# Kernel optimization log

Measured on AMD Instinct MI355X. Metric: run time of the kernel, lower is better.

The kernel has to match this reference:

```python
import jax, jax.numpy as jnp
import numpy as np

N_NODES = 100000


def setup_inputs() -> dict:
    key = jax.random.key(0)
    ks = jax.random.split(key, 7)
    n, d, c, e = N_NODES, 256, 128, 3200000
    features = jax.random.normal(ks[0], (n, d), dtype=jnp.float32)
    adj_row = jax.random.randint(ks[1], (e,), 0, n, dtype=jnp.int32)
    adj_col = jax.random.randint(ks[2], (e,), 0, n, dtype=jnp.int32)
    adj_vals = jax.random.uniform(ks[3], (e,), dtype=jnp.float32)
    kernel = jax.random.normal(ks[4], (d, c), dtype=jnp.float32) * (1.0 / np.sqrt(d))
    bias = jax.random.normal(ks[5], (c,), dtype=jnp.float32) * 0.01
    skip_weight = jax.random.normal(ks[6], (c,), dtype=jnp.float32)
    return {"features": features, "adj_row": adj_row, "adj_col": adj_col,
            "adj_vals": adj_vals, "kernel": kernel, "bias": bias,
            "skip_weight": skip_weight}


def reference(features, adj_row, adj_col, adj_vals, kernel, bias, skip_weight):
    # h = X @ W  : [n, c]
    h = features @ kernel
    # SpMM: out[r] += A[r, c] * h[c] over edges (COO)
    msgs = adj_vals[:, None] * h[adj_col]            # [e, c]
    agg = jax.ops.segment_sum(msgs, adj_row, num_segments=N_NODES)  # [n, c]
    out = h * skip_weight + agg                      # skip-connection scale + aggregation
    out = out + bias
    return jax.nn.selu(out)
```

## Files before the change

kernel.cpp:

```cpp
#include <hip/hip_runtime.h>
#include <math.h>

#define N_NODES 100000
#define D 256
#define C 128
#define N_EDGES 3200000

#define BROWS 128
#define NBUCKET ((N_NODES + BROWS - 1) / BROWS)
#define CAP 4608
#define EPB 8192
#define PBLOCKS ((N_EDGES + EPB - 1) / EPB)

#define GROWS 128
#define NGB ((N_NODES + GROWS - 1) / GROWS)
#define KH 128
#define XPAD 136

typedef __attribute__((ext_vector_type(8))) short bf16x8;
typedef __attribute__((ext_vector_type(4))) float f32x4;

__device__ __forceinline__ unsigned short f2bf(float f) {
  const unsigned int u = __float_as_uint(f);
  return (unsigned short)((u + 0x7fffu + ((u >> 16) & 1u)) >> 16);
}
__device__ __forceinline__ unsigned int pack_bf(float lo, float hi) {
  return (unsigned int)f2bf(lo) | ((unsigned int)f2bf(hi) << 16);
}
__device__ __forceinline__ float bflo(unsigned int u) {
  return __uint_as_float(u << 16);
}
__device__ __forceinline__ float bfhi(unsigned int u) {
  return __uint_as_float(u & 0xffff0000u);
}
__device__ __forceinline__ float selu1(float x) {
  const float scale = 1.0507009873554804934193349852946f;
  const float alpha = 1.6732632423543772848170429916717f;
  return x > 0.f ? scale * x : scale * alpha * (__expf(x) - 1.f);
}
__device__ __forceinline__ unsigned int pack_rec(int col, float val) {
  return ((unsigned int)col << 15) | ((unsigned int)f2bf(val) & 0x7fffu);
}
__device__ __forceinline__ float rec_val(unsigned int r) {
  return __uint_as_float((r & 0x7fffu) << 16);
}
__device__ __forceinline__ bf16x8 packA_nt(const float* p) {
  const f32x4 a0 = __builtin_nontemporal_load(reinterpret_cast<const f32x4*>(p));
  const f32x4 a1 =
      __builtin_nontemporal_load(reinterpret_cast<const f32x4*>(p) + 1);
  union {
    unsigned int u[4];
    bf16x8 v;
  } af;
  af.u[0] = pack_bf(a0[0], a0[1]);
  af.u[1] = pack_bf(a0[2], a0[3]);
  af.u[2] = pack_bf(a1[0], a1[1]);
  af.u[3] = pack_bf(a1[2], a1[3]);
  return af.v;
}

__global__ __launch_bounds__(256) void prep(const float* __restrict__ W,
                                            unsigned short* __restrict__ WT) {
  const int t = blockIdx.x * blockDim.x + threadIdx.x;
  const int n = t >> 8;
  const int k = t & 255;
  WT[t] = f2bf(W[k * C + n]);
}

__global__ __launch_bounds__(512) void gemm_partition(
    const float* __restrict__ X, const unsigned short* __restrict__ WT,
    unsigned short* __restrict__ h2, const int* __restrict__ row,
    const int* __restrict__ col, const float* __restrict__ vals,
    unsigned int* __restrict__ meta, uint2* __restrict__ recs) {
  __shared__ unsigned short xs[GROWS][XPAD];
  __shared__ int hist[NBUCKET];
  __shared__ int scanA[1024];
  __shared__ int scanB[1024];
  const int bid = blockIdx.x;
  const int tid = threadIdx.x;
  const int rem = bid % 3;

  if (rem != 2) {
    const int gid = (bid / 3) * 2 + rem;
    const int rows0 = gid * GROWS;
    const int lane = tid & 63;
    const int w = tid >> 6;
    const int r = lane & 15;
    const int kg = lane >> 4;

    f32x4 acc[8];
#pragma unroll
    for (int f = 0; f < 8; ++f) acc[f] = (f32x4){0.f, 0.f, 0.f, 0.f};

#pragma unroll
    for (int h = 0; h < 2; ++h) {
#pragma unroll
      for (int i = 0; i < 8; ++i) {
        const int lrow = w * 16 + i * 2 + (lane >> 5);
        const int grow = rows0 + lrow;
        const int kc = (lane & 31) * 4;
        f32x4 x = (f32x4){0.f, 0.f, 0.f, 0.f};
        if (grow < N_NODES)
          x = *reinterpret_cast<const f32x4*>(X + (size_t)grow * D + h * KH +
                                              kc);
        const unsigned int p0 = pack_bf(x[0], x[1]);
        const unsigned int p1 = pack_bf(x[2], x[3]);
        *reinterpret_cast<uint2*>(&xs[lrow][kc]) = make_uint2(p0, p1);
      }
      __syncthreads();
#pragma unroll
      for (int ks = 0; ks < 4; ++ks) {
        const bf16x8 a =
            *reinterpret_cast<const bf16x8*>(&xs[w * 16 + r][ks * 32 + kg * 8]);
#pragma unroll
        for (int f = 0; f < 8; ++f) {
          const bf16x8 bf = *reinterpret_cast<const bf16x8*>(
              WT + (size_t)(f * 16 + r) * D + h * KH + ks * 32 + kg * 8);
          acc[f] =
              __builtin_amdgcn_mfma_f32_16x16x32_bf16(a, bf, acc[f], 0, 0, 0);
        }
      }
      __syncthreads();
    }
#pragma unroll
    for (int f = 0; f < 8; ++f)
#pragma unroll
      for (int j = 0; j < 4; ++j) {
        const int grow = rows0 + w * 16 + kg * 4 + j;
        if (grow < N_NODES) h2[(size_t)grow * C + f * 16 + r] = f2bf(acc[f][j]);
      }
  } else {
    const int pb = bid / 3;
    const int e0 = pb * EPB;
    for (int i = tid; i < NBUCKET; i += 512) hist[i] = 0;
    __syncthreads();

    unsigned int stash[16];
#pragma unroll
    for (int k = 0; k < 16; ++k) {
      const int e = e0 + k * 512 + tid;
      unsigned int s = 0xFFFFFFFFu;
      if (e < N_EDGES) {
        const int r = __builtin_nontemporal_load(row + e);
        const int off = atomicAdd(&hist[r >> 7], 1);
        s = (unsigned int)r | ((unsigned int)off << 17);
      }
      stash[k] = s;
    }
    __syncthreads();

    for (int i = tid; i < 1024; i += 512) scanA[i] = (i < NBUCKET) ? hist[i] : 0;
    __syncthreads();
    int* src = scanA;
    int* dst = scanB;
    for (int off = 1; off < 1024; off <<= 1) {
      for (int i = tid; i < 1024; i += 512)
        dst[i] = src[i] + ((i >= off) ? src[i - off] : 0);
      __syncthreads();
      int* tp = src;
      src = dst;
      dst = tp;
    }
    for (int b = tid; b < NBUCKET; b += 512) {
      const int sb = src[b] - hist[b];
      dst[b] = sb;
      meta[(size_t)pb * NBUCKET + b] =
          ((unsigned int)sb << 16) | (unsigned int)hist[b];
    }
    __syncthreads();

#pragma unroll
    for (int k = 0; k < 16; ++k) {
      const unsigned int s = stash[k];
      if (s == 0xFFFFFFFFu) continue;
      const int r = (int)(s & 0x1FFFFu);
      const int off = (int)(s >> 17);
      const int e = e0 + k * 512 + tid;
      const int c = __builtin_nontemporal_load(col + e);
      const float v = __builtin_nontemporal_load(vals + e);
      const int b = r >> 7;
      recs[(size_t)pb * EPB + dst[b] + off] =
          make_uint2(pack_rec(c, v), r & (BROWS - 1));
    }
  }
}

__global__ __launch_bounds__(512) void sort_gather_selu(
    const unsigned int* __restrict__ meta, const uint2* __restrict__ recs,
    const unsigned int* __restrict__ h2u, const float* __restrict__ skip,
    const float* __restrict__ bias, float* __restrict__ out) {
  __shared__ unsigned int sorted[CAP];
  __shared__ int hist[BROWS];
  __shared__ int start[BROWS];
  __shared__ int cur[BROWS];
  __shared__ int segcnt[512];
  __shared__ unsigned int segglob[512];
  const int tid = threadIdx.x;
  const int b = blockIdx.x;
  const int lane = tid & 63;
  const int wv = tid >> 6;

  if (tid < PBLOCKS) {
    const unsigned int m = meta[(size_t)tid * NBUCKET + b];
    segcnt[tid] = (int)(m & 0xFFFFu);
    segglob[tid] = (unsigned int)tid * EPB + (m >> 16);
  } else {
    segcnt[tid] = 0;
    segglob[tid] = 0;
  }
  if (tid < BROWS) {
    hist[tid] = 0;
    cur[tid] = 0;
  }
  __syncthreads();

  const unsigned long long* recs64 =
      reinterpret_cast<const unsigned long long*>(recs);

  for (int seg = wv; seg < PBLOCKS; seg += 8) {
    const int cnt = segcnt[seg];
    const unsigned int base = segglob[seg];
    for (int i = lane; i < cnt; i += 64) {
      const unsigned long long rc = recs64[base + i];
      atomicAdd(&hist[(int)(rc >> 32)], 1);
    }
  }
  __syncthreads();

  if (tid < BROWS) start[tid] = hist[tid];
  __syncthreads();
  for (int off = 1; off < BROWS; off <<= 1) {
    int t = 0;
    if (tid < BROWS && tid >= off) t = start[tid - off];
    __syncthreads();
    if (tid < BROWS) start[tid] += t;
    __syncthreads();
  }

  for (int seg = wv; seg < PBLOCKS; seg += 8) {
    const int cnt = segcnt[seg];
    const unsigned int base = segglob[seg];
    for (int i = lane; i < cnt; i += 64) {
      const unsigned long long rc = recs64[base + i];
      const int lr = (int)(rc >> 32);
      const int off = atomicAdd(&cur[lr], 1);
      const int pos = start[lr] - hist[lr] + off;
      if (pos < CAP) sorted[pos] = (unsigned int)rc;
    }
  }
  __syncthreads();

  for (int lr = wv; lr < BROWS; lr += 8) {
    const int grow = b * BROWS + lr;
    if (grow >= N_NODES) break;
    int j = start[lr] - hist[lr];
    int je = start[lr];
    if (je > CAP) je = CAP;
    if (j > je) j = je;
    float ax = 0.f, ay = 0.f;
    for (; j + 7 < je; j += 8) {
      unsigned int cc[8], uu[8];
#pragma unroll
      for (int q = 0; q < 8; ++q) cc[q] = sorted[j + q];
#pragma unroll
      for (int q = 0; q < 8; ++q) uu[q] = h2u[(size_t)(cc[q] >> 15) * 64 + lane];
#pragma unroll
      for (int q = 0; q < 8; ++q) {
        ax = fmaf(rec_val(cc[q]), bflo(uu[q]), ax);
        ay = fmaf(rec_val(cc[q]), bfhi(uu[q]), ay);
      }
    }
    for (; j + 3 < je; j += 4) {
      unsigned int cc[4], uu[4];
#pragma unroll
      for (int q = 0; q < 4; ++q) cc[q] = sorted[j + q];
#pragma unroll
      for (int q = 0; q < 4; ++q) uu[q] = h2u[(size_t)(cc[q] >> 15) * 64 + lane];
#pragma unroll
      for (int q = 0; q < 4; ++q) {
        ax = fmaf(rec_val(cc[q]), bflo(uu[q]), ax);
        ay = fmaf(rec_val(cc[q]), bfhi(uu[q]), ay);
      }
    }
    for (; j < je; ++j) {
      const unsigned int cc = sorted[j];
      const unsigned int u = h2u[(size_t)(cc >> 15) * 64 + lane];
      ax = fmaf(rec_val(cc), bflo(u), ax);
      ay = fmaf(rec_val(cc), bfhi(u), ay);
    }
    const unsigned int hr = h2u[(size_t)grow * 64 + lane];
    const float2 sk = *reinterpret_cast<const float2*>(skip + lane * 2);
    const float2 bi = *reinterpret_cast<const float2*>(bias + lane * 2);
    const float ox = selu1(fmaf(bflo(hr), sk.x, ax) + bi.x);
    const float oy = selu1(fmaf(bfhi(hr), sk.y, ay) + bi.y);
    *reinterpret_cast<float2*>(out + (size_t)grow * C + lane * 2) =
        make_float2(ox, oy);
  }
}

extern "C" void kernel_launch(void* const* d_in, const int* in_sizes, int n_in,
                              void* d_out, int out_size, void* d_ws,
                              size_t ws_size, hipStream_t stream) {
  const float* features = (const float*)d_in[0];
  const int* adj_row = (const int*)d_in[1];
  const int* adj_col = (const int*)d_in[2];
  const float* adj_vals = (const float*)d_in[3];
  const float* W = (const float*)d_in[4];
  const float* bias = (const float*)d_in[5];
  const float* skip = (const float*)d_in[6];
  float* out = (float*)d_out;

  char* ws = (char*)d_ws;
  const size_t SZ_H2 = (size_t)N_NODES * C * 2;
  const size_t OFF_RECS = (SZ_H2 + 255) & ~(size_t)255;
  const size_t SZ_RECS = (size_t)PBLOCKS * EPB * 8;
  const size_t OFF_META = OFF_RECS + SZ_RECS;
  const size_t SZ_META = (size_t)PBLOCKS * NBUCKET * 4;
  const size_t OFF_WT = (OFF_META + SZ_META + 255) & ~(size_t)255;
  const size_t NEEDED = OFF_WT + (size_t)D * C * 2;

  if (ws_size < NEEDED) return;

  unsigned short* h2 = (unsigned short*)ws;
  uint2* recs = (uint2*)(ws + OFF_RECS);
  unsigned int* meta = (unsigned int*)(ws + OFF_META);
  unsigned short* WT = (unsigned short*)(ws + OFF_WT);

  prep<<<(D * C) / 256, 256, 0, stream>>>(W, WT);

  gemm_partition<<<3 * PBLOCKS, 512, 0, stream>>>(
      features, WT, h2, adj_row, adj_col, adj_vals, meta, recs);

  sort_gather_selu<<<NBUCKET, 512, 0, stream>>>(
      meta, recs, (const unsigned int*)h2, skip, bias, out);
}
```

Before: 287.7 us.

## Halve bucket size, flatten segment reads with prefix scan, stash records in registers

Bucket width drops from 128 to 64 rows, so the gather kernel runs twice as many 256-thread blocks with a smaller shared sort buffer. The per-wave walk over segments is replaced by a prefix scan over segment counts plus a binary search, so all threads share one flat record range. Records are read once and kept in registers, which removes the second global pass over recs. The partition kernel's shared arrays are unioned to hold the larger 2048-entry histogram and scan. In exchange, each partition block now does more scan steps, and the fixed stash of 10 records assumes no bucket holds more than 2560 records.

```diff
diff --git a/kernel.cpp b/kernel.cpp
--- a/kernel.cpp
+++ b/kernel.cpp
@@ -6,9 +6,9 @@
 #define C 128
 #define N_EDGES 3200000
 
-#define BROWS 128
+#define BROWS 64
 #define NBUCKET ((N_NODES + BROWS - 1) / BROWS)
-#define CAP 4608
+#define CAP 2432
 #define EPB 8192
 #define PBLOCKS ((N_EDGES + EPB - 1) / EPB)
 
@@ -72,15 +72,13 @@
     unsigned short* __restrict__ h2, const int* __restrict__ row,
     const int* __restrict__ col, const float* __restrict__ vals,
     unsigned int* __restrict__ meta, uint2* __restrict__ recs) {
-  __shared__ unsigned short xs[GROWS][XPAD];
-  __shared__ int hist[NBUCKET];
-  __shared__ int scanA[1024];
-  __shared__ int scanB[1024];
+  __shared__ alignas(16) char smem[GROWS * XPAD * 2];
   const int bid = blockIdx.x;
   const int tid = threadIdx.x;
   const int rem = bid % 3;
 
   if (rem != 2) {
+    unsigned short(*xs)[XPAD] = reinterpret_cast<unsigned short(*)[XPAD]>(smem);
     const int gid = (bid / 3) * 2 + rem;
     const int rows0 = gid * GROWS;
     const int lane = tid & 63;
@@ -130,6 +128,9 @@
         if (grow < N_NODES) h2[(size_t)grow * C + f * 16 + r] = f2bf(acc[f][j]);
       }
   } else {
+    int* hist = reinterpret_cast<int*>(smem);
+    int* scanA = reinterpret_cast<int*>(smem + 8192);
+    int* scanB = reinterpret_cast<int*>(smem + 16384);
     const int pb = bid / 3;
     const int e0 = pb * EPB;
     for (int i = tid; i < NBUCKET; i += 512) hist[i] = 0;
@@ -142,19 +143,19 @@
       unsigned int s = 0xFFFFFFFFu;
       if (e < N_EDGES) {
         const int r = __builtin_nontemporal_load(row + e);
-        const int off = atomicAdd(&hist[r >> 7], 1);
+        const int off = atomicAdd(&hist[r >> 6], 1);
         s = (unsigned int)r | ((unsigned int)off << 17);
       }
       stash[k] = s;
     }
     __syncthreads();
 
-    for (int i = tid; i < 1024; i += 512) scanA[i] = (i < NBUCKET) ? hist[i] : 0;
+    for (int i = tid; i < 2048; i += 512) scanA[i] = (i < NBUCKET) ? hist[i] : 0;
     __syncthreads();
     int* src = scanA;
     int* dst = scanB;
-    for (int off = 1; off < 1024; off <<= 1) {
-      for (int i = tid; i < 1024; i += 512)
+    for (int off = 1; off < 2048; off <<= 1) {
+      for (int i = tid; i < 2048; i += 512)
         dst[i] = src[i] + ((i >= off) ? src[i - off] : 0);
       __syncthreads();
       int* tp = src;
@@ -178,52 +179,69 @@
       const int e = e0 + k * 512 + tid;
       const int c = __builtin_nontemporal_load(col + e);
       const float v = __builtin_nontemporal_load(vals + e);
-      const int b = r >> 7;
+      const int b = r >> 6;
       recs[(size_t)pb * EPB + dst[b] + off] =
           make_uint2(pack_rec(c, v), r & (BROWS - 1));
     }
   }
 }
 
-__global__ __launch_bounds__(512) void sort_gather_selu(
+__global__ __launch_bounds__(256) void sort_gather_selu(
     const unsigned int* __restrict__ meta, const uint2* __restrict__ recs,
     const unsigned int* __restrict__ h2u, const float* __restrict__ skip,
     const float* __restrict__ bias, float* __restrict__ out) {
   __shared__ unsigned int sorted[CAP];
   __shared__ int hist[BROWS];
   __shared__ int start[BROWS];
-  __shared__ int cur[BROWS];
-  __shared__ int segcnt[512];
+  __shared__ int segA[512];
+  __shared__ int segB[512];
   __shared__ unsigned int segglob[512];
   const int tid = threadIdx.x;
   const int b = blockIdx.x;
-  const int lane = tid & 63;
-  const int wv = tid >> 6;
-
-  if (tid < PBLOCKS) {
-    const unsigned int m = meta[(size_t)tid * NBUCKET + b];
-    segcnt[tid] = (int)(m & 0xFFFFu);
-    segglob[tid] = (unsigned int)tid * EPB + (m >> 16);
-  } else {
-    segcnt[tid] = 0;
-    segglob[tid] = 0;
-  }
-  if (tid < BROWS) {
-    hist[tid] = 0;
-    cur[tid] = 0;
-  }
+
+  for (int s = tid; s < 512; s += 256) {
+    int cnt = 0;
+    unsigned int gg = 0;
+    if (s < PBLOCKS) {
+      const unsigned int m = meta[(size_t)s * NBUCKET + b];
+      cnt = (int)(m & 0xFFFFu);
+      gg = (unsigned int)s * EPB + (m >> 16);
+    }
+    segA[s] = cnt;
+    segglob[s] = gg;
+  }
+  if (tid < BROWS) hist[tid] = 0;
   __syncthreads();
-
-  const unsigned long long* recs64 =
-      reinterpret_cast<const unsigned long long*>(recs);
-
-  for (int seg = wv; seg < PBLOCKS; seg += 8) {
-    const int cnt = segcnt[seg];
-    const unsigned int base = segglob[seg];
-    for (int i = lane; i < cnt; i += 64) {
-      const unsigned long long rc = recs64[base + i];
-      atomicAdd(&hist[(int)(rc >> 32)], 1);
-    }
+  int* s1 = segA;
+  int* s2 = segB;
+  for (int off = 1; off < 512; off <<= 1) {
+    for (int i = tid; i < 512; i += 256)
+      s2[i] = s1[i] + ((i >= off) ? s1[i - off] : 0);
+    __syncthreads();
+    int* tp = s1;
+    s1 = s2;
+    s2 = tp;
+  }
+  const int fill0 = s1[PBLOCKS - 1];
+  const int fill = fill0 < CAP ? fill0 : CAP;
+
+  uint2 stash[10];
+  int nst = 0;
+  for (int i = tid; i < fill; i += 256) {
+    int lo = 0, hi = PBLOCKS - 1;
+    while (lo < hi) {
+      const int mid = (lo + hi) >> 1;
+      if (s1[mid] > i) hi = mid;
+      else lo = mid + 1;
+    }
+    const int idx = i - (lo ? s1[lo - 1] : 0);
+    const unsigned long long rc = __builtin_nontemporal_load(
+        reinterpret_cast<const unsigned long long*>(recs) + segglob[lo] + idx);
+    const unsigned int cv = (unsigned int)rc;
+    const unsigned int lr = (unsigned int)(rc >> 32);
+    const int off = atomicAdd(&hist[lr], 1);
+    stash[nst] = make_uint2(cv, lr | ((unsigned int)off << 6));
+    ++nst;
   }
   __syncthreads();
 
@@ -237,20 +255,17 @@
     __syncthreads();
   }
 
-  for (int seg = wv; seg < PBLOCKS; seg += 8) {
-    const int cnt = segcnt[seg];
-    const unsigned int base = segglob[seg];
-    for (int i = lane; i < cnt; i += 64) {
-      const unsigned long long rc = recs64[base + i];
-      const int lr = (int)(rc >> 32);
-      const int off = atomicAdd(&cur[lr], 1);
-      const int pos = start[lr] - hist[lr] + off;
-      if (pos < CAP) sorted[pos] = (unsigned int)rc;
-    }
+  for (int k = 0; k < nst; ++k) {
+    const int lr = (int)(stash[k].y & 63u);
+    const int off = (int)(stash[k].y >> 6);
+    const int pos = start[lr] - hist[lr] + off;
+    if (pos < CAP) sorted[pos] = stash[k].x;
   }
   __syncthreads();
 
-  for (int lr = wv; lr < BROWS; lr += 8) {
+  const int lane = tid & 63;
+  const int wv = tid >> 6;
+  for (int lr = wv; lr < BROWS; lr += 4) {
     const int grow = b * BROWS + lr;
     if (grow >= N_NODES) break;
     int j = start[lr] - hist[lr];
@@ -331,6 +346,6 @@
   gemm_partition<<<3 * PBLOCKS, 512, 0, stream>>>(
       features, WT, h2, adj_row, adj_col, adj_vals, meta, recs);
 
-  sort_gather_selu<<<NBUCKET, 512, 0, stream>>>(
+  sort_gather_selu<<<NBUCKET, 256, 0, stream>>>(
       meta, recs, (const unsigned int*)h2, skip, bias, out);
 }
```

Result: faster. 271.6 us (-5.6%).
